# Optimization experiments

Hardware: AMD Instinct MI355X
Metric: run time of the kernel (lower is better)

Reference implementation:

```python
import jax, jax.numpy as jnp
import numpy as np

B, U, D, N, O = 128, 16, 256, 1024, 256
RES_CONN, IN_CONN, BIAS_P = 0.2, 0.2, 0.5


def _fixed_bernoulli(rng, heads, rows, cols, conn):
    # each column has exactly nb = int(conn*rows) ones (as in the torch code)
    nb = max(1, int(conn * rows))
    r = rng.random((heads, rows, cols))
    thr = np.sort(r, axis=1)[:, nb - 1:nb, :]
    return (r <= thr).astype(np.float32)


def setup_inputs() -> dict:
    rng = np.random.default_rng(0)
    # recurrent weights: normal * fixed-bernoulli mask, normalized by spectral radius
    W = rng.normal(size=(U, N, N)).astype(np.float32) * _fixed_bernoulli(rng, U, N, N, RES_CONN)
    sr0 = np.abs(np.linalg.eigvals(W.astype(np.float64))).max(axis=-1).astype(np.float32).reshape(U, 1, 1)
    W = W / sr0
    Win = _fixed_bernoulli(rng, U, D, N, IN_CONN)
    bias = (rng.random((U, 1, N)) < BIAS_P).astype(np.float32)
    Wout = rng.normal(size=(U, N, O)).astype(np.float32)
    adaptive_lr = rng.random((U, D, 1)).astype(np.float32)
    sr = rng.random((U, 1, 1)).astype(np.float32)
    temperature = np.ones((1,), np.float32)
    X = rng.normal(size=(B, U, D)).astype(np.float32)
    state = rng.normal(size=(B, U, N)).astype(np.float32)
    arrs = dict(X=X, state=state, W=W, Win=Win, bias=bias, Wout=Wout,
                sr=sr, adaptive_lr=adaptive_lr, temperature=temperature)
    return {k: jnp.asarray(v) for k, v in arrs.items()}


def reference(X, state, W, Win, bias, Wout, sr, adaptive_lr, temperature):
    # X: [B,U,D] -> [B,U,1,D]; state: [B,U,N] -> [B,U,1,N]
    x = X[:, :, None, :]
    s = state[:, :, None, :]
    # adaptive per-unit learning rate: softmax over the units axis
    lr = jax.nn.softmax(jnp.einsum('buid,udk->buik', x, adaptive_lr) / temperature, axis=1)  # [B,U,1,1]
    feed = jnp.einsum('buid,udn->buin', x, Win)            # [B,U,1,N]
    echo = jnp.einsum('buin,unm->buim', s, W * sr) + bias  # [B,U,1,N]
    new_state = (1.0 - lr) * s + lr * jnp.tanh(feed + echo)
    output = jnp.einsum('buin,uno->buio', new_state, Wout)  # [B,U,1,O]
    return new_state[:, :, 0, :], output[:, :, 0, :]
```

## Files before the change

kernel.cpp:

```cpp
#include <hip/hip_runtime.h>
#include <math.h>

#define Bsz 128
#define Usz 16
#define Dsz 256
#define Nsz 1024
#define Osz 256
#define BK  64

typedef __attribute__((ext_vector_type(2))) unsigned int u32x2;
typedef __attribute__((ext_vector_type(4))) unsigned int u32x4;
typedef __attribute__((ext_vector_type(4))) float f32x4;
typedef __attribute__((ext_vector_type(8))) short bf16x8;

union cell_u { u32x4 u; bf16x8 b; };

__device__ __forceinline__ unsigned int fbits(float f) {
    union { float f; unsigned int u; } v; v.f = f; return v.u;
}
__device__ __forceinline__ unsigned int pk(float lo, float hi) {
    return __builtin_amdgcn_perm(fbits(hi), fbits(lo), 0x07060302u);
}
__device__ __forceinline__ u32x2 pk4(f32x4 v, float s) {
    v *= s;
    u32x2 r; r[0] = pk(v[0], v[1]); r[1] = pk(v[2], v[3]);
    return r;
}
__device__ __forceinline__ bf16x8 ldB8(const float* p, size_t str) {
    const float x0 = p[0],       x1 = p[str],     x2 = p[2*str], x3 = p[3*str];
    const float x4 = p[4*str],   x5 = p[5*str],   x6 = p[6*str], x7 = p[7*str];
    cell_u r;
    r.u[0] = pk(x0, x1); r.u[1] = pk(x2, x3);
    r.u[2] = pk(x4, x5); r.u[3] = pk(x6, x7);
    return r.b;
}

__device__ __forceinline__ void sync_nodrain() {
    __builtin_amdgcn_sched_barrier(0);
    asm volatile("s_waitcnt lgkmcnt(0)");
    __builtin_amdgcn_sched_barrier(0);
    __builtin_amdgcn_s_barrier();
    __builtin_amdgcn_sched_barrier(0);
}

__global__ __launch_bounds__(256)
void lr_kernel(const float* __restrict__ X, const float* __restrict__ alr,
               const float* __restrict__ temp, float* __restrict__ lr)
{
    const int b = blockIdx.x;
    const int t = threadIdx.x;
    const int u = t >> 4;
    const int l = t & 15;
    const float* xp = X + ((size_t)b * Usz + u) * Dsz;
    const float* ap = alr + (size_t)u * Dsz;
    float s = 0.f;
    for (int d = l; d < Dsz; d += 16) s += xp[d] * ap[d];
    s += __shfl_down(s, 8, 16);
    s += __shfl_down(s, 4, 16);
    s += __shfl_down(s, 2, 16);
    s += __shfl_down(s, 1, 16);
    __shared__ float logits[16];
    if (l == 0) logits[u] = s;
    __syncthreads();
    if (t < 16) {
        const float T = temp[0];
        float m = -1e30f;
        #pragma unroll
        for (int i = 0; i < 16; i++) m = fmaxf(m, logits[i] / T);
        float sum = 0.f;
        #pragma unroll
        for (int i = 0; i < 16; i++) sum += expf(logits[i] / T - m);
        lr[(size_t)b * Usz + t] = expf(logits[t] / T - m) / sum;
    }
}

__global__ __launch_bounds__(256)
void state_gemm(const float* __restrict__ X, const float* __restrict__ state,
                const float* __restrict__ W, const float* __restrict__ Win,
                const float* __restrict__ bias, const float* __restrict__ sr,
                const float* __restrict__ lr, float* __restrict__ out0)
{
    const int id = blockIdx.x;
    const int u  = id & 15;
    const int nt = id >> 4;

    const int tid  = threadIdx.x;
    const int wave = tid >> 6, lane = tid & 63;
    const int l16  = lane & 15, kgl = lane >> 4;
    const int wm = wave & 1, wn = wave >> 1;

    __shared__ unsigned short As[2][128 * 72];

    const float sru = sr[u];

    const int r0 = tid >> 4;
    const int c  = tid & 15;

    f32x4 raE[8], raO[8];

    auto ldA = [&](int s, f32x4 (&ra)[8]) {
        const int k0 = s * BK;
        if (k0 < Dsz) {
            const float* base = X + ((size_t)r0 * Usz + u) * Dsz + k0 + c * 4;
            #pragma unroll
            for (int i = 0; i < 8; i++)
                ra[i] = *(const f32x4*)(base + (size_t)16 * i * Usz * Dsz);
        } else {
            const float* base = state + ((size_t)r0 * Usz + u) * Nsz + (k0 - Dsz) + c * 4;
            #pragma unroll
            for (int i = 0; i < 8; i++)
                ra[i] = *(const f32x4*)(base + (size_t)16 * i * Usz * Nsz);
        }
    };
    auto wrA = [&](int p, f32x4 (&ra)[8], float sc) {
        #pragma unroll
        for (int i = 0; i < 8; i++)
            *(u32x2*)&As[p][(r0 + 16 * i) * 72 + c * 4] = pk4(ra[i], sc);
    };

    const int col = nt * 32 + wn * 16 + l16;

    cell_u rb0[2], rb1[2];
    auto ldBf = [&](int s, cell_u rb[2]) {
        const int k0 = s * BK;
        const float* bbase = (k0 < Dsz)
            ? Win + (size_t)u * Dsz * Nsz + (size_t)k0 * Nsz
            : W   + (size_t)u * Nsz * Nsz + (size_t)(k0 - Dsz) * Nsz;
        #pragma unroll
        for (int kk = 0; kk < 2; kk++)
            rb[kk].b = ldB8(bbase + (size_t)(kk * 32 + kgl * 8) * Nsz + col, Nsz);
    };

    f32x4 acc[4] = {};
    auto comp = [&](int p, cell_u rb[2]) {
        #pragma unroll
        for (int kk = 0; kk < 2; kk++) {
            #pragma unroll
            for (int mi = 0; mi < 4; mi++) {
                const bf16x8 af = *(const bf16x8*)&As[p][(wm * 64 + mi * 16 + l16) * 72 + kk * 32 + kgl * 8];
                acc[mi] = __builtin_amdgcn_mfma_f32_16x16x32_bf16(af, rb[kk].b, acc[mi], 0, 0, 0);
            }
        }
    };

    ldA(0, raO);
    ldBf(0, rb0);
    ldA(1, raE);
    wrA(0, raO, 1.f);
    sync_nodrain();

    for (int s2 = 0; s2 < 10; s2++) {
        const int s = 2 * s2;
        ldBf(s + 1, rb1);
        if (s + 2 < 20) ldA(s + 2, raO);
        wrA(1, raE, (s + 1 < 4) ? 1.f : sru);
        comp(0, rb0);
        sync_nodrain();
        if (s + 2 < 20) {
            ldBf(s + 2, rb0);
            if (s + 3 < 20) ldA(s + 3, raE);
            wrA(0, raO, (s + 2 < 4) ? 1.f : sru);
        }
        comp(1, rb1);
        sync_nodrain();
    }

    const int gcol = nt * 32 + wn * 16 + l16;
    const float bi = bias[u * Nsz + gcol];
    #pragma unroll
    for (int mi = 0; mi < 4; mi++) {
        #pragma unroll
        for (int rg = 0; rg < 4; rg++) {
            const int grow = wm * 64 + mi * 16 + kgl * 4 + rg;
            const size_t idx = ((size_t)grow * Usz + u) * Nsz + gcol;
            const float th = tanhf(acc[mi][rg] + bi);
            const float lv = lr[grow * Usz + u];
            out0[idx] = (1.f - lv) * state[idx] + lv * th;
        }
    }
}

__global__ __launch_bounds__(256)
void out_gemm(const float* __restrict__ ns, const float* __restrict__ Wout,
              float* __restrict__ dst, int nsteps, int partial)
{
    const int id = blockIdx.x;
    const int u  = id & 15;
    const int ot = (id >> 4) & 7;
    const int ks = id >> 7;
    const int kbase = ks * nsteps * BK;

    const int tid  = threadIdx.x;
    const int wave = tid >> 6, lane = tid & 63;
    const int l16  = lane & 15, kgl = lane >> 4;
    const int wm = wave & 1, wn = wave >> 1;

    __shared__ unsigned short As[2][128 * 72];

    const int r0 = tid >> 4;
    const int c  = tid & 15;

    f32x4 raE[8], raO[8];
    auto ldA = [&](int s, f32x4 (&ra)[8]) {
        const float* base = ns + ((size_t)r0 * Usz + u) * Nsz + kbase + s * BK + c * 4;
        #pragma unroll
        for (int i = 0; i < 8; i++)
            ra[i] = *(const f32x4*)(base + (size_t)16 * i * Usz * Nsz);
    };
    auto wrA = [&](int p, f32x4 (&ra)[8]) {
        #pragma unroll
        for (int i = 0; i < 8; i++)
            *(u32x2*)&As[p][(r0 + 16 * i) * 72 + c * 4] = pk4(ra[i], 1.f);
    };

    const int col = ot * 32 + wn * 16 + l16;

    cell_u rb0[2], rb1[2];
    auto ldBf = [&](int s, cell_u rb[2]) {
        const float* bbase = Wout + (size_t)u * Nsz * Osz + (size_t)(kbase + s * BK) * Osz;
        #pragma unroll
        for (int kk = 0; kk < 2; kk++)
            rb[kk].b = ldB8(bbase + (size_t)(kk * 32 + kgl * 8) * Osz + col, Osz);
    };

    f32x4 acc[4] = {};
    auto comp = [&](int p, cell_u rb[2]) {
        #pragma unroll
        for (int kk = 0; kk < 2; kk++) {
            #pragma unroll
            for (int mi = 0; mi < 4; mi++) {
                const bf16x8 af = *(const bf16x8*)&As[p][(wm * 64 + mi * 16 + l16) * 72 + kk * 32 + kgl * 8];
                acc[mi] = __builtin_amdgcn_mfma_f32_16x16x32_bf16(af, rb[kk].b, acc[mi], 0, 0, 0);
            }
        }
    };

    ldA(0, raO);
    ldBf(0, rb0);
    ldA(1, raE);
    wrA(0, raO);
    sync_nodrain();

    for (int s2 = 0; s2 < nsteps / 2; s2++) {
        const int s = 2 * s2;
        ldBf(s + 1, rb1);
        if (s + 2 < nsteps) ldA(s + 2, raO);
        wrA(1, raE);
        comp(0, rb0);
        sync_nodrain();
        if (s + 2 < nsteps) {
            ldBf(s + 2, rb0);
            if (s + 3 < nsteps) ldA(s + 3, raE);
            wrA(0, raO);
        }
        comp(1, rb1);
        sync_nodrain();
    }

    const int gcol = ot * 32 + wn * 16 + l16;
    #pragma unroll
    for (int mi = 0; mi < 4; mi++) {
        #pragma unroll
        for (int rg = 0; rg < 4; rg++) {
            const int grow = wm * 64 + mi * 16 + kgl * 4 + rg;
            if (partial)
                dst[(((size_t)ks * 16 + u) * 128 + grow) * 256 + gcol] = acc[mi][rg];
            else
                dst[((size_t)grow * Usz + u) * Osz + gcol] = acc[mi][rg];
        }
    }
}

__global__ __launch_bounds__(256)
void out_reduce(const float* __restrict__ part, float* __restrict__ out1)
{
    const size_t i = (size_t)blockIdx.x * 256 + threadIdx.x;
    const size_t base = i * 4;
    const int m = (int)(base >> 12);
    const int u = (int)((base >> 8) & 15);
    const int o = (int)(base & 255);

    const size_t pb = ((size_t)u * 128 + m) * 256 + o;
    const size_t slab = (size_t)16 * 128 * 256;
    f32x4 s = *(const f32x4*)(part + pb);
    s += *(const f32x4*)(part + pb + slab);
    s += *(const f32x4*)(part + pb + 2 * slab);
    s += *(const f32x4*)(part + pb + 3 * slab);
    *(f32x4*)(out1 + base) = s;
}

extern "C" void kernel_launch(void* const* d_in, const int* in_sizes, int n_in,
                              void* d_out, int out_size, void* d_ws, size_t ws_size,
                              hipStream_t stream)
{
    (void)in_sizes; (void)n_in; (void)out_size;
    const float* X     = (const float*)d_in[0];
    const float* state = (const float*)d_in[1];
    const float* W     = (const float*)d_in[2];
    const float* Win   = (const float*)d_in[3];
    const float* bias  = (const float*)d_in[4];
    const float* Wout  = (const float*)d_in[5];
    const float* sr    = (const float*)d_in[6];
    const float* alr   = (const float*)d_in[7];
    const float* temp  = (const float*)d_in[8];

    float* out0 = (float*)d_out;
    float* out1 = out0 + (size_t)Bsz * Usz * Nsz;
    float* lr   = (float*)d_ws;

    const size_t p_off   = 8192;
    const size_t p_bytes = (size_t)4 * 16 * 128 * 256 * 4;

    lr_kernel<<<Bsz, 256, 0, stream>>>(X, alr, temp, lr);
    state_gemm<<<512, 256, 0, stream>>>(X, state, W, Win, bias, sr, lr, out0);

    if (ws_size >= p_off + p_bytes) {
        float* part = (float*)((char*)d_ws + p_off);
        out_gemm<<<512, 256, 0, stream>>>(out0, Wout, part, 4, 1);
        out_reduce<<<512, 256, 0, stream>>>(part, out1);
    } else {
        out_gemm<<<128, 256, 0, stream>>>(out0, Wout, out1, 16, 0);
    }
}
```

Baseline: 182.2 us.

## Stage B tiles through LDS with coalesced loads and split M across blocks

In both GEMM kernels, B operands are now loaded as coalesced float4 rows and transposed into an LDS tile. Previously each lane gathered eight strided scalars from global memory. The M dimension is split into two 64-row tiles, doubling the grid to raise parallelism, and block ids are reordered so tiles of the same unit sit next to each other. The lr kernel also switches to vectorized float4 loads. The scalar 16-bit transposed LDS stores may cause bank conflicts, and the A tile from X/state is now reloaded by twice as many blocks.

```diff
diff --git a/kernel.cpp b/kernel.cpp
--- a/kernel.cpp
+++ b/kernel.cpp
@@ -7,32 +7,21 @@
 #define Nsz 1024
 #define Osz 256
 #define BK  64
+#define LDT 72
 
 typedef __attribute__((ext_vector_type(2))) unsigned int u32x2;
 typedef __attribute__((ext_vector_type(4))) unsigned int u32x4;
 typedef __attribute__((ext_vector_type(4))) float f32x4;
 typedef __attribute__((ext_vector_type(8))) short bf16x8;
 
-union cell_u { u32x4 u; bf16x8 b; };
-
 __device__ __forceinline__ unsigned int fbits(float f) {
     union { float f; unsigned int u; } v; v.f = f; return v.u;
 }
 __device__ __forceinline__ unsigned int pk(float lo, float hi) {
     return __builtin_amdgcn_perm(fbits(hi), fbits(lo), 0x07060302u);
 }
-__device__ __forceinline__ u32x2 pk4(f32x4 v, float s) {
-    v *= s;
-    u32x2 r; r[0] = pk(v[0], v[1]); r[1] = pk(v[2], v[3]);
-    return r;
-}
-__device__ __forceinline__ bf16x8 ldB8(const float* p, size_t str) {
-    const float x0 = p[0],       x1 = p[str],     x2 = p[2*str], x3 = p[3*str];
-    const float x4 = p[4*str],   x5 = p[5*str],   x6 = p[6*str], x7 = p[7*str];
-    cell_u r;
-    r.u[0] = pk(x0, x1); r.u[1] = pk(x2, x3);
-    r.u[2] = pk(x4, x5); r.u[3] = pk(x6, x7);
-    return r.b;
+__device__ __forceinline__ unsigned short bf16t(float f) {
+    return (unsigned short)(fbits(f) >> 16);
 }
 
 __device__ __forceinline__ void sync_nodrain() {
@@ -51,10 +40,14 @@
     const int t = threadIdx.x;
     const int u = t >> 4;
     const int l = t & 15;
-    const float* xp = X + ((size_t)b * Usz + u) * Dsz;
-    const float* ap = alr + (size_t)u * Dsz;
+    const f32x4* xp = (const f32x4*)(X + ((size_t)b * Usz + u) * Dsz + l * 16);
+    const f32x4* ap = (const f32x4*)(alr + (size_t)u * Dsz + l * 16);
     float s = 0.f;
-    for (int d = l; d < Dsz; d += 16) s += xp[d] * ap[d];
+    #pragma unroll
+    for (int j = 0; j < 4; j++) {
+        const f32x4 xv = xp[j], av = ap[j];
+        s += xv[0]*av[0] + xv[1]*av[1] + xv[2]*av[2] + xv[3]*av[3];
+    }
     s += __shfl_down(s, 8, 16);
     s += __shfl_down(s, 4, 16);
     s += __shfl_down(s, 2, 16);
@@ -81,97 +74,98 @@
                 const float* __restrict__ lr, float* __restrict__ out0)
 {
     const int id = blockIdx.x;
-    const int u  = id & 15;
-    const int nt = id >> 4;
+    const int nt = id & 31;
+    const int u  = (id >> 5) & 15;
+    const int mt = id >> 9;
 
     const int tid  = threadIdx.x;
     const int wave = tid >> 6, lane = tid & 63;
     const int l16  = lane & 15, kgl = lane >> 4;
     const int wm = wave & 1, wn = wave >> 1;
 
-    __shared__ unsigned short As[2][128 * 72];
+    __shared__ unsigned short As[2][64 * LDT];
+    __shared__ unsigned short Bs[2][32 * LDT];
 
     const float sru = sr[u];
 
-    const int r0 = tid >> 4;
-    const int c  = tid & 15;
-
-    f32x4 raE[8], raO[8];
-
-    auto ldA = [&](int s, f32x4 (&ra)[8]) {
+    const int rA = tid >> 2;
+    const int cA = (tid & 3) * 16;
+    const int kB = tid >> 3;
+    const int nB = (tid & 7) * 4;
+    const int col0 = nt * 32;
+
+    f32x4 rAE[4], rAO[4];
+    f32x4 rBE[2], rBO[2];
+
+    auto ldA = [&](int s, f32x4 (&ra)[4]) {
         const int k0 = s * BK;
-        if (k0 < Dsz) {
-            const float* base = X + ((size_t)r0 * Usz + u) * Dsz + k0 + c * 4;
+        const float* base = (k0 < Dsz)
+            ? X     + (((size_t)(mt * 64 + rA) * Usz + u) * Dsz) + k0 + cA
+            : state + (((size_t)(mt * 64 + rA) * Usz + u) * Nsz) + (k0 - Dsz) + cA;
+        #pragma unroll
+        for (int j = 0; j < 4; j++) ra[j] = *(const f32x4*)(base + 4 * j);
+    };
+    auto ldB = [&](int s, f32x4 (&rb)[2]) {
+        const int k0 = s * BK;
+        const float* base = (k0 < Dsz)
+            ? Win + (size_t)u * Dsz * Nsz + (size_t)(k0 + kB) * Nsz + col0 + nB
+            : W   + (size_t)u * Nsz * Nsz + (size_t)(k0 - Dsz + kB) * Nsz + col0 + nB;
+        rb[0] = *(const f32x4*)base;
+        rb[1] = *(const f32x4*)(base + (size_t)32 * Nsz);
+    };
+    auto wrA = [&](int p, f32x4 (&ra)[4]) {
+        #pragma unroll
+        for (int j = 0; j < 4; j++) {
+            u32x2 w; w[0] = pk(ra[j][0], ra[j][1]); w[1] = pk(ra[j][2], ra[j][3]);
+            *(u32x2*)&As[p][rA * LDT + cA + 4 * j] = w;
+        }
+    };
+    auto wrB = [&](int p, f32x4 (&rb)[2], float sc) {
+        #pragma unroll
+        for (int h = 0; h < 2; h++)
             #pragma unroll
-            for (int i = 0; i < 8; i++)
-                ra[i] = *(const f32x4*)(base + (size_t)16 * i * Usz * Dsz);
-        } else {
-            const float* base = state + ((size_t)r0 * Usz + u) * Nsz + (k0 - Dsz) + c * 4;
+            for (int j = 0; j < 4; j++)
+                Bs[p][(nB + j) * LDT + kB + 32 * h] = bf16t(rb[h][j] * sc);
+    };
+
+    f32x4 acc[2] = {};
+    auto comp = [&](int p) {
+        #pragma unroll
+        for (int kk = 0; kk < 2; kk++) {
+            const bf16x8 bf = *(const bf16x8*)&Bs[p][(wn * 16 + l16) * LDT + kk * 32 + kgl * 8];
             #pragma unroll
-            for (int i = 0; i < 8; i++)
-                ra[i] = *(const f32x4*)(base + (size_t)16 * i * Usz * Nsz);
-        }
-    };
-    auto wrA = [&](int p, f32x4 (&ra)[8], float sc) {
-        #pragma unroll
-        for (int i = 0; i < 8; i++)
-            *(u32x2*)&As[p][(r0 + 16 * i) * 72 + c * 4] = pk4(ra[i], sc);
-    };
-
-    const int col = nt * 32 + wn * 16 + l16;
-
-    cell_u rb0[2], rb1[2];
-    auto ldBf = [&](int s, cell_u rb[2]) {
-        const int k0 = s * BK;
-        const float* bbase = (k0 < Dsz)
-            ? Win + (size_t)u * Dsz * Nsz + (size_t)k0 * Nsz
-            : W   + (size_t)u * Nsz * Nsz + (size_t)(k0 - Dsz) * Nsz;
-        #pragma unroll
-        for (int kk = 0; kk < 2; kk++)
-            rb[kk].b = ldB8(bbase + (size_t)(kk * 32 + kgl * 8) * Nsz + col, Nsz);
-    };
-
-    f32x4 acc[4] = {};
-    auto comp = [&](int p, cell_u rb[2]) {
-        #pragma unroll
-        for (int kk = 0; kk < 2; kk++) {
-            #pragma unroll
-            for (int mi = 0; mi < 4; mi++) {
-                const bf16x8 af = *(const bf16x8*)&As[p][(wm * 64 + mi * 16 + l16) * 72 + kk * 32 + kgl * 8];
-                acc[mi] = __builtin_amdgcn_mfma_f32_16x16x32_bf16(af, rb[kk].b, acc[mi], 0, 0, 0);
+            for (int mi = 0; mi < 2; mi++) {
+                const bf16x8 af = *(const bf16x8*)&As[p][(wm * 32 + mi * 16 + l16) * LDT + kk * 32 + kgl * 8];
+                acc[mi] = __builtin_amdgcn_mfma_f32_16x16x32_bf16(af, bf, acc[mi], 0, 0, 0);
             }
         }
     };
-
-    ldA(0, raO);
-    ldBf(0, rb0);
-    ldA(1, raE);
-    wrA(0, raO, 1.f);
+    auto scB = [&](int s) -> float { return (s * BK < Dsz) ? 1.f : sru; };
+
+    ldA(0, rAE); ldB(0, rBE);
+    ldA(1, rAO); ldB(1, rBO);
+    wrA(0, rAE); wrB(0, rBE, scB(0));
     sync_nodrain();
 
     for (int s2 = 0; s2 < 10; s2++) {
         const int s = 2 * s2;
-        ldBf(s + 1, rb1);
-        if (s + 2 < 20) ldA(s + 2, raO);
-        wrA(1, raE, (s + 1 < 4) ? 1.f : sru);
-        comp(0, rb0);
+        if (s + 2 < 20) { ldA(s + 2, rAE); ldB(s + 2, rBE); }
+        wrA(1, rAO); wrB(1, rBO, scB(s + 1));
+        comp(0);
         sync_nodrain();
-        if (s + 2 < 20) {
-            ldBf(s + 2, rb0);
-            if (s + 3 < 20) ldA(s + 3, raE);
-            wrA(0, raO, (s + 2 < 4) ? 1.f : sru);
-        }
-        comp(1, rb1);
+        if (s + 3 < 20) { ldA(s + 3, rAO); ldB(s + 3, rBO); }
+        if (s + 2 < 20) { wrA(0, rAE); wrB(0, rBE, scB(s + 2)); }
+        comp(1);
         sync_nodrain();
     }
 
     const int gcol = nt * 32 + wn * 16 + l16;
     const float bi = bias[u * Nsz + gcol];
     #pragma unroll
-    for (int mi = 0; mi < 4; mi++) {
+    for (int mi = 0; mi < 2; mi++) {
         #pragma unroll
         for (int rg = 0; rg < 4; rg++) {
-            const int grow = wm * 64 + mi * 16 + kgl * 4 + rg;
+            const int grow = mt * 64 + wm * 32 + mi * 16 + kgl * 4 + rg;
             const size_t idx = ((size_t)grow * Usz + u) * Nsz + gcol;
             const float th = tanhf(acc[mi][rg] + bi);
             const float lv = lr[grow * Usz + u];
@@ -185,9 +179,10 @@
               float* __restrict__ dst, int nsteps, int partial)
 {
     const int id = blockIdx.x;
-    const int u  = id & 15;
-    const int ot = (id >> 4) & 7;
-    const int ks = id >> 7;
+    const int ot = id & 7;
+    const int u  = (id >> 3) & 15;
+    const int mt = (id >> 7) & 1;
+    const int ks = id >> 8;
     const int kbase = ks * nsteps * BK;
 
     const int tid  = threadIdx.x;
@@ -195,74 +190,80 @@
     const int l16  = lane & 15, kgl = lane >> 4;
     const int wm = wave & 1, wn = wave >> 1;
 
-    __shared__ unsigned short As[2][128 * 72];
-
-    const int r0 = tid >> 4;
-    const int c  = tid & 15;
-
-    f32x4 raE[8], raO[8];
-    auto ldA = [&](int s, f32x4 (&ra)[8]) {
-        const float* base = ns + ((size_t)r0 * Usz + u) * Nsz + kbase + s * BK + c * 4;
-        #pragma unroll
-        for (int i = 0; i < 8; i++)
-            ra[i] = *(const f32x4*)(base + (size_t)16 * i * Usz * Nsz);
-    };
-    auto wrA = [&](int p, f32x4 (&ra)[8]) {
-        #pragma unroll
-        for (int i = 0; i < 8; i++)
-            *(u32x2*)&As[p][(r0 + 16 * i) * 72 + c * 4] = pk4(ra[i], 1.f);
-    };
-
-    const int col = ot * 32 + wn * 16 + l16;
-
-    cell_u rb0[2], rb1[2];
-    auto ldBf = [&](int s, cell_u rb[2]) {
-        const float* bbase = Wout + (size_t)u * Nsz * Osz + (size_t)(kbase + s * BK) * Osz;
-        #pragma unroll
-        for (int kk = 0; kk < 2; kk++)
-            rb[kk].b = ldB8(bbase + (size_t)(kk * 32 + kgl * 8) * Osz + col, Osz);
-    };
-
-    f32x4 acc[4] = {};
-    auto comp = [&](int p, cell_u rb[2]) {
+    __shared__ unsigned short As[2][64 * LDT];
+    __shared__ unsigned short Bs[2][32 * LDT];
+
+    const int rA = tid >> 2;
+    const int cA = (tid & 3) * 16;
+    const int kB = tid >> 3;
+    const int nB = (tid & 7) * 4;
+    const int col0 = ot * 32;
+
+    f32x4 rAE[4], rAO[4];
+    f32x4 rBE[2], rBO[2];
+
+    auto ldA = [&](int s, f32x4 (&ra)[4]) {
+        const float* base = ns + (((size_t)(mt * 64 + rA) * Usz + u) * Nsz) + kbase + s * BK + cA;
+        #pragma unroll
+        for (int j = 0; j < 4; j++) ra[j] = *(const f32x4*)(base + 4 * j);
+    };
+    auto ldB = [&](int s, f32x4 (&rb)[2]) {
+        const float* base = Wout + (size_t)u * Nsz * Osz
+                          + (size_t)(kbase + s * BK + kB) * Osz + col0 + nB;
+        rb[0] = *(const f32x4*)base;
+        rb[1] = *(const f32x4*)(base + (size_t)32 * Osz);
+    };
+    auto wrA = [&](int p, f32x4 (&ra)[4]) {
+        #pragma unroll
+        for (int j = 0; j < 4; j++) {
+            u32x2 w; w[0] = pk(ra[j][0], ra[j][1]); w[1] = pk(ra[j][2], ra[j][3]);
+            *(u32x2*)&As[p][rA * LDT + cA + 4 * j] = w;
+        }
+    };
+    auto wrB = [&](int p, f32x4 (&rb)[2]) {
+        #pragma unroll
+        for (int h = 0; h < 2; h++)
+            #pragma unroll
+            for (int j = 0; j < 4; j++)
+                Bs[p][(nB + j) * LDT + kB + 32 * h] = bf16t(rb[h][j]);
+    };
+
+    f32x4 acc[2] = {};
+    auto comp = [&](int p) {
         #pragma unroll
         for (int kk = 0; kk < 2; kk++) {
+            const bf16x8 bf = *(const bf16x8*)&Bs[p][(wn * 16 + l16) * LDT + kk * 32 + kgl * 8];
             #pragma unroll
-            for (int mi = 0; mi < 4; mi++) {
-                const bf16x8 af = *(const bf16x8*)&As[p][(wm * 64 + mi * 16 + l16) * 72 + kk * 32 + kgl * 8];
-                acc[mi] = __builtin_amdgcn_mfma_f32_16x16x32_bf16(af, rb[kk].b, acc[mi], 0, 0, 0);
+            for (int mi = 0; mi < 2; mi++) {
+                const bf16x8 af = *(const bf16x8*)&As[p][(wm * 32 + mi * 16 + l16) * LDT + kk * 32 + kgl * 8];
+                acc[mi] = __builtin_amdgcn_mfma_f32_16x16x32_bf16(af, bf, acc[mi], 0, 0, 0);
             }
         }
     };
 
-    ldA(0, raO);
-    ldBf(0, rb0);
-    ldA(1, raE);
-    wrA(0, raO);
+    ldA(0, rAE); ldB(0, rBE);
+    ldA(1, rAO); ldB(1, rBO);
+    wrA(0, rAE); wrB(0, rBE);
     sync_nodrain();
 
     for (int s2 = 0; s2 < nsteps / 2; s2++) {
         const int s = 2 * s2;
-        ldBf(s + 1, rb1);
-        if (s + 2 < nsteps) ldA(s + 2, raO);
-        wrA(1, raE);
-        comp(0, rb0);
+        if (s + 2 < nsteps) { ldA(s + 2, rAE); ldB(s + 2, rBE); }
+        wrA(1, rAO); wrB(1, rBO);
+        comp(0);
         sync_nodrain();
-        if (s + 2 < nsteps) {
-            ldBf(s + 2, rb0);
-            if (s + 3 < nsteps) ldA(s + 3, raE);
-            wrA(0, raO);
-        }
-        comp(1, rb1);
+        if (s + 3 < nsteps) { ldA(s + 3, rAO); ldB(s + 3, rBO); }
+        if (s + 2 < nsteps) { wrA(0, rAE); wrB(0, rBE); }
+        comp(1);
         sync_nodrain();
     }
 
     const int gcol = ot * 32 + wn * 16 + l16;
     #pragma unroll
-    for (int mi = 0; mi < 4; mi++) {
+    for (int mi = 0; mi < 2; mi++) {
         #pragma unroll
         for (int rg = 0; rg < 4; rg++) {
-            const int grow = wm * 64 + mi * 16 + kgl * 4 + rg;
+            const int grow = mt * 64 + wm * 32 + mi * 16 + kgl * 4 + rg;
             if (partial)
                 dst[(((size_t)ks * 16 + u) * 128 + grow) * 256 + gcol] = acc[mi][rg];
             else
@@ -312,13 +313,13 @@
     const size_t p_bytes = (size_t)4 * 16 * 128 * 256 * 4;
 
     lr_kernel<<<Bsz, 256, 0, stream>>>(X, alr, temp, lr);
-    state_gemm<<<512, 256, 0, stream>>>(X, state, W, Win, bias, sr, lr, out0);
+    state_gemm<<<1024, 256, 0, stream>>>(X, state, W, Win, bias, sr, lr, out0);
 
     if (ws_size >= p_off + p_bytes) {
         float* part = (float*)((char*)d_ws + p_off);
-        out_gemm<<<512, 256, 0, stream>>>(out0, Wout, part, 4, 1);
+        out_gemm<<<1024, 256, 0, stream>>>(out0, Wout, part, 4, 1);
         out_reduce<<<512, 256, 0, stream>>>(part, out1);
     } else {
-        out_gemm<<<128, 256, 0, stream>>>(out0, Wout, out1, 16, 0);
-    }
-}
+        out_gemm<<<256, 256, 0, stream>>>(out0, Wout, out1, 16, 0);
+    }
+}
```

New measurement: 194.2 us. 6.6% more time.
